# Performance work log

Measured on AMD Instinct MI355X. Metric: run time of the kernel, lower is better.

## Reference

```python
import jax, jax.numpy as jnp
import numpy as np
import math

B, C_IN, C_OUT, K, H = 4, 128, 128, 3, 16
A = C_IN // 8  # attn_dim = in_channels // 8 per 'individual' mode


def setup_inputs() -> dict:
    key = jax.random.key(0)
    ks = jax.random.split(key, 8)
    s = 0.02
    return {
        "x": jax.random.normal(ks[0], (B, C_IN, H, H), jnp.float32),
        "weight": jax.random.normal(ks[1], (C_OUT, C_IN, K, K), jnp.float32) * s,
        "fc_q_w": jax.random.normal(ks[2], (A, C_IN), jnp.float32) * s,
        "fc_q_b": jnp.zeros((A,), jnp.float32),
        "fc_k_w": jax.random.normal(ks[3], (A, 1), jnp.float32) * s,
        "fc_k_b": jnp.zeros((A,), jnp.float32),
        "fc_v_w": jax.random.normal(ks[4], (A, 1), jnp.float32) * s,
        "fc_v_b": jnp.zeros((A,), jnp.float32),
        "fc_o_w": jax.random.normal(ks[5], (1, A), jnp.float32) * s,
        "fc_o_b": jnp.zeros((1,), jnp.float32),
        "gamma": jax.random.normal(ks[6], (1,), jnp.float32),
    }


def reference(x, weight, fc_q_w, fc_q_b, fc_k_w, fc_k_b, fc_v_w, fc_v_b,
              fc_o_w, fc_o_b, gamma):
    b, c_in, h, w_sp = x.shape
    c_out, _, kh, kw = weight.shape
    wflat = weight.reshape(-1)                                 # [Wn]
    xt = x.reshape(b, c_in, -1).transpose(0, 2, 1)             # [B, HW, C_in]
    # AttnOverWeight (mode='individual')
    q = xt @ fc_q_w.T + fc_q_b                                 # [B, HW, A]
    k = wflat[:, None] * fc_k_w[:, 0][None, :] + fc_k_b        # [Wn, A] (Linear(1,A))
    v = wflat[:, None] * fc_v_w[:, 0][None, :] + fc_v_b        # [Wn, A]
    scores = jnp.einsum('bqa,na->bqn', q, k) / math.sqrt(q.shape[-1])
    attn = jax.nn.softmax(scores, axis=2)                      # [B, HW, Wn]
    attn_out = attn.mean(axis=1)[:, :, None] * v[None]         # [B, Wn, A]
    weighted_w = (attn_out @ fc_o_w.T + fc_o_b)[..., 0]        # [B, Wn]
    masked_w = wflat[None, :] + gamma * weighted_w             # [B, Wn]
    # per-sample conv via grouped conv (groups = batch)
    kernels = masked_w.reshape(b * c_out, c_in, kh, kw)
    xg = x.reshape(1, b * c_in, h, w_sp)
    out = jax.lax.conv_general_dilated(
        xg, kernels, window_strides=(1, 1), padding=[(1, 1), (1, 1)],
        feature_group_count=b, dimension_numbers=('NCHW', 'OIHW', 'NCHW'))
    return out.reshape(b, c_out, out.shape[2], out.shape[3])
```

## Files before the change

kernel.cpp:

```cpp
#include <hip/hip_runtime.h>

#define B_      4
#define CIN     128
#define COUT    128
#define HW      256
#define WN      147456
#define WPK     1152
#define ADIM    16

#define WS_G     0
#define WS_G0    128
#define WS_S1    129
#define WS_S0    130
#define WS_BO    131
#define WS_A     132
#define WS_PART  160
#define NBLK_MOM 144
#define MWT_OFF  4096
#define XT_OFF   (4096 + 4*9*128*128*2)

typedef __attribute__((ext_vector_type(8))) short bf16x8;
typedef __attribute__((ext_vector_type(4))) float f32x4;

__device__ __forceinline__ unsigned short f2bf(float f) {
    union { float f; unsigned int u; } v; v.f = f;
    unsigned int u = v.u;
    return (unsigned short)((u + 0x7FFFu + ((u >> 16) & 1u)) >> 16);
}

__device__ __forceinline__ float waveReduceSum(float v) {
    #pragma unroll
    for (int off = 32; off; off >>= 1) v += __shfl_down(v, off, 64);
    return v;
}

__device__ __forceinline__ float blockSum256(float v, float* tmp4, int tid) {
    v = waveReduceSum(v);
    __syncthreads();
    if ((tid & 63) == 0) tmp4[tid >> 6] = v;
    __syncthreads();
    return tmp4[0] + tmp4[1] + tmp4[2] + tmp4[3];
}

__device__ __forceinline__ float blockSum1024(float v, float* tmp16, int tid) {
    v = waveReduceSum(v);
    __syncthreads();
    if ((tid & 63) == 0) tmp16[tid >> 6] = v;
    __syncthreads();
    float s = 0.f;
    #pragma unroll
    for (int i = 0; i < 16; ++i) s += tmp16[i];
    return s;
}

__global__ __launch_bounds__(256) void k_moments(
        const float* __restrict__ w,
        const float* __restrict__ fcq,  const float* __restrict__ fcqb,
        const float* __restrict__ fck,
        const float* __restrict__ fcv,  const float* __restrict__ fcvb,
        const float* __restrict__ fco,  const float* __restrict__ fcob,
        float* __restrict__ ws) {
    __shared__ float tmp4[4];
    const int tid = threadIdx.x, blk = blockIdx.x;

    const float4 w4 = *reinterpret_cast<const float4*>(w + (size_t)(blk * 256 + tid) * 4);
    float m0 = 0.f, m1 = 0.f, m2 = 0.f, m3 = 0.f, m4 = 0.f, m5 = 0.f;
    float vals[4] = {w4.x, w4.y, w4.z, w4.w};
    #pragma unroll
    for (int i = 0; i < 4; ++i) {
        float v = vals[i], v2 = v * v, v3 = v2 * v;
        m0 += v; m1 += v2; m2 += v3; m3 += v2 * v2; m4 += v2 * v3; m5 += v3 * v3;
    }
    float ms[6] = {m0, m1, m2, m3, m4, m5};
    #pragma unroll
    for (int k = 0; k < 6; ++k) {
        float s = blockSum256(ms[k], tmp4, tid);
        if (tid == 0) ws[WS_PART + blk * 6 + k] = s;
    }
    if (blk == 0) {
        if (tid < 128) {
            float s = 0.f;
            #pragma unroll
            for (int a = 0; a < ADIM; ++a) s += fcq[a * CIN + tid] * fck[a];
            ws[WS_G + tid] = s;
        } else if (tid == 128) {
            float s = 0.f;
            for (int a = 0; a < ADIM; ++a) s += fcqb[a] * fck[a];
            ws[WS_G0] = s;
        } else if (tid == 129) {
            float s = 0.f;
            for (int a = 0; a < ADIM; ++a) s += fcv[a] * fco[a];
            ws[WS_S1] = s;
        } else if (tid == 130) {
            float s = 0.f;
            for (int a = 0; a < ADIM; ++a) s += fcvb[a] * fco[a];
            ws[WS_S0] = s;
        } else if (tid == 131) {
            ws[WS_BO] = fcob[0];
        }
    }
}

__global__ __launch_bounds__(1024) void k_alpha(
        const float* __restrict__ x, float* __restrict__ ws) {
    __shared__ float tmp16[16];
    __shared__ float S[7];
    __shared__ float gl[128];
    __shared__ float g0s;
    __shared__ float psum[4][256];
    const int tid = threadIdx.x, b = blockIdx.x;
    const int p = tid & 255, cg = tid >> 8;

    #pragma unroll
    for (int k = 0; k < 6; ++k) {
        float v = (tid < NBLK_MOM) ? ws[WS_PART + tid * 6 + k] : 0.f;
        float s = blockSum1024(v, tmp16, tid);
        if (tid == 0) S[k + 1] = s;
    }
    if (tid < 128) gl[tid] = ws[WS_G + tid];
    if (tid == 128) g0s = ws[WS_G0];
    __syncthreads();

    float dot = 0.f;
    const float* xb = x + (size_t)b * CIN * HW + p;
    const int c0 = cg * 32;
    #pragma unroll 8
    for (int c = 0; c < 32; ++c) dot += xb[(c0 + c) * HW] * gl[c0 + c];
    psum[cg][p] = dot;
    __syncthreads();

    float alpha = 0.f, r = 0.f;
    if (cg == 0) {
        alpha = (psum[0][p] + psum[1][p] + psum[2][p] + psum[3][p] + g0s) * 0.25f;
        float Z = S[6] * (1.f / 720.f);
        Z = Z * alpha + S[5] * (1.f / 120.f);
        Z = Z * alpha + S[4] * (1.f / 24.f);
        Z = Z * alpha + S[3] * (1.f / 6.f);
        Z = Z * alpha + S[2] * 0.5f;
        Z = Z * alpha + S[1];
        Z = Z * alpha + (float)WN;
        r = 1.0f / ((float)HW * Z);
    }
    float t = r;
    const float invk[7] = {1.f, 1.f, 0.5f, 1.f / 3.f, 0.25f, 0.2f, 1.f / 6.f};
    #pragma unroll
    for (int k = 0; k < 7; ++k) {
        float s = blockSum1024(t, tmp16, tid);
        if (tid == 0) ws[WS_A + b * 7 + k] = s;
        t = t * alpha * invk[k + 1 > 6 ? 6 : k + 1];
    }
}

__global__ __launch_bounds__(256) void k_mask(
        const float* __restrict__ w, const float* __restrict__ ws,
        const float* __restrict__ gamma, unsigned short* __restrict__ mwT) {
    const int b = blockIdx.x >> 3, chunk = blockIdx.x & 7;
    const float A0 = ws[WS_A + b * 7 + 0], A1 = ws[WS_A + b * 7 + 1];
    const float A2 = ws[WS_A + b * 7 + 2], A3 = ws[WS_A + b * 7 + 3];
    const float A4 = ws[WS_A + b * 7 + 4], A5 = ws[WS_A + b * 7 + 5];
    const float A6 = ws[WS_A + b * 7 + 6];
    const float s1 = ws[WS_S1], s0 = ws[WS_S0], bo = ws[WS_BO];
    const float gam = gamma[0];

    const int end = chunk * 2048 + 2048;
    for (int i = chunk * 2048 + threadIdx.x; i < end; i += 256) {
        const int co = i >> 7, ci = i & 127;
        const float* wp = w + co * WPK + ci * 9;
        #pragma unroll
        for (int j = 0; j < 9; ++j) {
            float wv = wp[j];
            float pp = A6;
            pp = pp * wv + A5; pp = pp * wv + A4; pp = pp * wv + A3;
            pp = pp * wv + A2; pp = pp * wv + A1; pp = pp * wv + A0;
            float mwv = wv + gam * (pp * (s1 * wv + s0) + bo);
            mwT[(((b * 9 + j) << 7 | co) << 7) | ci] = f2bf(mwv);
        }
    }
}

__global__ __launch_bounds__(256) void k_xt(
        const float* __restrict__ x, unsigned short* __restrict__ xT) {
    const int b = blockIdx.x, tid = threadIdx.x;
    if (tid < 68) {
        int rr, cc;
        if (tid < 18)      { rr = 0;            cc = tid; }
        else if (tid < 36) { rr = 17;           cc = tid - 18; }
        else if (tid < 52) { rr = tid - 36 + 1; cc = 0; }
        else               { rr = tid - 52 + 1; cc = 17; }
        unsigned short* dst = xT + ((size_t)b * 324 + rr * 18 + cc) * 128;
        bf16x8 z = {};
        #pragma unroll
        for (int i = 0; i < 16; ++i) *reinterpret_cast<bf16x8*>(dst + i * 8) = z;
    }
    const int py = tid >> 4, px = tid & 15;
    const float* xb = x + (size_t)b * CIN * HW + tid;
    unsigned short* dst = xT + ((size_t)b * 324 + (py + 1) * 18 + (px + 1)) * 128;
    for (int ci0 = 0; ci0 < 128; ci0 += 8) {
        bf16x8 pk;
        #pragma unroll
        for (int e = 0; e < 8; ++e) pk[e] = (short)f2bf(xb[(ci0 + e) * HW]);
        *reinterpret_cast<bf16x8*>(dst + ci0) = pk;
    }
}

__global__ __launch_bounds__(64) void k_conv_mfma(
        const unsigned short* __restrict__ mwT,
        const unsigned short* __restrict__ xT,
        float* __restrict__ out) {
    const int wgid = blockIdx.x;
    const int l = threadIdx.x;
    const int b = wgid >> 5;
    const int rem = wgid & 31;
    const int cobase = (rem >> 3) * 32;
    const int pbase  = (rem & 7) * 32;
    const int lr = l & 15, lk = l >> 4;

    const int p0 = pbase + lr,       p1 = pbase + 16 + lr;
    const int py0 = p0 >> 4, px0 = p0 & 15;
    const int py1 = p1 >> 4, px1 = p1 & 15;

    f32x4 acc[2][2] = {};

    #pragma unroll 1
    for (int j = 0; j < 9; ++j) {
        const int dy = j / 3, dx = j % 3;
        const unsigned short* ab = mwT + (((b * 9 + j) * 128 + cobase + lr) * 128 + lk * 8);
        const unsigned short* bb0 = xT + (((size_t)b * 324 + (py0 + dy) * 18 + (px0 + dx)) * 128 + lk * 8);
        const unsigned short* bb1 = xT + (((size_t)b * 324 + (py1 + dy) * 18 + (px1 + dx)) * 128 + lk * 8);
        #pragma unroll
        for (int c = 0; c < 4; ++c) {
            bf16x8 a0 = *reinterpret_cast<const bf16x8*>(ab + c * 32);
            bf16x8 a1 = *reinterpret_cast<const bf16x8*>(ab + 16 * 128 + c * 32);
            bf16x8 vb0 = *reinterpret_cast<const bf16x8*>(bb0 + c * 32);
            bf16x8 vb1 = *reinterpret_cast<const bf16x8*>(bb1 + c * 32);
            acc[0][0] = __builtin_amdgcn_mfma_f32_16x16x32_bf16(a0, vb0, acc[0][0], 0, 0, 0);
            acc[0][1] = __builtin_amdgcn_mfma_f32_16x16x32_bf16(a0, vb1, acc[0][1], 0, 0, 0);
            acc[1][0] = __builtin_amdgcn_mfma_f32_16x16x32_bf16(a1, vb0, acc[1][0], 0, 0, 0);
            acc[1][1] = __builtin_amdgcn_mfma_f32_16x16x32_bf16(a1, vb1, acc[1][1], 0, 0, 0);
        }
    }
    #pragma unroll
    for (int s = 0; s < 2; ++s)
        #pragma unroll
        for (int t = 0; t < 2; ++t)
            #pragma unroll
            for (int r = 0; r < 4; ++r) {
                const int co = cobase + s * 16 + lk * 4 + r;
                const int p  = pbase + t * 16 + lr;
                out[((size_t)b * COUT + co) * HW + p] = acc[s][t][r];
            }
}

extern "C" void kernel_launch(void* const* d_in, const int* in_sizes, int n_in,
                              void* d_out, int out_size, void* d_ws, size_t ws_size,
                              hipStream_t stream) {
    const float* x    = (const float*)d_in[0];
    const float* wt   = (const float*)d_in[1];
    const float* fcq  = (const float*)d_in[2];
    const float* fcqb = (const float*)d_in[3];
    const float* fck  = (const float*)d_in[4];
    const float* fcv  = (const float*)d_in[6];
    const float* fcvb = (const float*)d_in[7];
    const float* fco  = (const float*)d_in[8];
    const float* fcob = (const float*)d_in[9];
    const float* gam  = (const float*)d_in[10];
    float* ws  = (float*)d_ws;
    unsigned short* mwT = (unsigned short*)((char*)d_ws + MWT_OFF);
    unsigned short* xT  = (unsigned short*)((char*)d_ws + XT_OFF);
    float* out = (float*)d_out;

    hipLaunchKernelGGL(k_moments, dim3(NBLK_MOM), dim3(256), 0, stream,
                       wt, fcq, fcqb, fck, fcv, fcvb, fco, fcob, ws);
    hipLaunchKernelGGL(k_alpha, dim3(B_), dim3(1024), 0, stream, x, ws);
    hipLaunchKernelGGL(k_mask, dim3(32), dim3(256), 0, stream, wt, ws, gam, mwT);
    hipLaunchKernelGGL(k_xt, dim3(B_), dim3(256), 0, stream, x, xT);
    hipLaunchKernelGGL(k_conv_mfma, dim3(128), dim3(64), 0, stream, mwT, xT, out);
}
```

Measured before the change: 107.4 us.

## Fuse moments into alpha kernel and merge mask/xT kernels to cut launches

Folds the weight moment reduction into the alpha kernel: each of the 4 batch blocks recomputes all moments over the full weight tensor itself instead of reading partials. The mask and input-transpose kernels are merged into one launch, so the pipeline drops from five launches to three. The conv loop over the 9 taps is also unrolled by 3. This removes launch gaps and global round-trips, at the cost of redundant 590KB weight reads in each of only 4 blocks, which serialises that reduction onto few CUs.

```diff
diff --git a/kernel.cpp b/kernel.cpp
--- a/kernel.cpp
+++ b/kernel.cpp
@@ -8,14 +8,10 @@
 #define WPK     1152
 #define ADIM    16
 
-#define WS_G     0
-#define WS_G0    128
-#define WS_S1    129
-#define WS_S0    130
-#define WS_BO    131
-#define WS_A     132
-#define WS_PART  160
-#define NBLK_MOM 144
+#define WS_A     0
+#define WS_S1    28
+#define WS_S0    29
+#define WS_BO    30
 #define MWT_OFF  4096
 #define XT_OFF   (4096 + 4*9*128*128*2)
 
@@ -34,14 +30,6 @@
     return v;
 }
 
-__device__ __forceinline__ float blockSum256(float v, float* tmp4, int tid) {
-    v = waveReduceSum(v);
-    __syncthreads();
-    if ((tid & 63) == 0) tmp4[tid >> 6] = v;
-    __syncthreads();
-    return tmp4[0] + tmp4[1] + tmp4[2] + tmp4[3];
-}
-
 __device__ __forceinline__ float blockSum1024(float v, float* tmp16, int tid) {
     v = waveReduceSum(v);
     __syncthreads();
@@ -53,74 +41,62 @@
     return s;
 }
 
-__global__ __launch_bounds__(256) void k_moments(
-        const float* __restrict__ w,
+__global__ __launch_bounds__(1024) void k_head(
+        const float* __restrict__ x, const float* __restrict__ w,
         const float* __restrict__ fcq,  const float* __restrict__ fcqb,
         const float* __restrict__ fck,
         const float* __restrict__ fcv,  const float* __restrict__ fcvb,
         const float* __restrict__ fco,  const float* __restrict__ fcob,
         float* __restrict__ ws) {
-    __shared__ float tmp4[4];
-    const int tid = threadIdx.x, blk = blockIdx.x;
-
-    const float4 w4 = *reinterpret_cast<const float4*>(w + (size_t)(blk * 256 + tid) * 4);
-    float m0 = 0.f, m1 = 0.f, m2 = 0.f, m3 = 0.f, m4 = 0.f, m5 = 0.f;
-    float vals[4] = {w4.x, w4.y, w4.z, w4.w};
-    #pragma unroll
-    for (int i = 0; i < 4; ++i) {
-        float v = vals[i], v2 = v * v, v3 = v2 * v;
-        m0 += v; m1 += v2; m2 += v3; m3 += v2 * v2; m4 += v2 * v3; m5 += v3 * v3;
-    }
-    float ms[6] = {m0, m1, m2, m3, m4, m5};
-    #pragma unroll
-    for (int k = 0; k < 6; ++k) {
-        float s = blockSum256(ms[k], tmp4, tid);
-        if (tid == 0) ws[WS_PART + blk * 6 + k] = s;
-    }
-    if (blk == 0) {
-        if (tid < 128) {
-            float s = 0.f;
-            #pragma unroll
-            for (int a = 0; a < ADIM; ++a) s += fcq[a * CIN + tid] * fck[a];
-            ws[WS_G + tid] = s;
-        } else if (tid == 128) {
-            float s = 0.f;
-            for (int a = 0; a < ADIM; ++a) s += fcqb[a] * fck[a];
-            ws[WS_G0] = s;
-        } else if (tid == 129) {
-            float s = 0.f;
-            for (int a = 0; a < ADIM; ++a) s += fcv[a] * fco[a];
-            ws[WS_S1] = s;
-        } else if (tid == 130) {
-            float s = 0.f;
-            for (int a = 0; a < ADIM; ++a) s += fcvb[a] * fco[a];
-            ws[WS_S0] = s;
-        } else if (tid == 131) {
-            ws[WS_BO] = fcob[0];
-        }
-    }
-}
-
-__global__ __launch_bounds__(1024) void k_alpha(
-        const float* __restrict__ x, float* __restrict__ ws) {
     __shared__ float tmp16[16];
     __shared__ float S[7];
     __shared__ float gl[128];
     __shared__ float g0s;
     __shared__ float psum[4][256];
     const int tid = threadIdx.x, b = blockIdx.x;
+
+    const float4* w4 = reinterpret_cast<const float4*>(w);
+    float m[6] = {0.f, 0.f, 0.f, 0.f, 0.f, 0.f};
+    #pragma unroll
+    for (int i = 0; i < 36; ++i) {
+        float4 v4 = w4[i * 1024 + tid];
+        float vals[4] = {v4.x, v4.y, v4.z, v4.w};
+        #pragma unroll
+        for (int e = 0; e < 4; ++e) {
+            float v = vals[e], v2 = v * v, v3 = v2 * v;
+            m[0] += v; m[1] += v2; m[2] += v3;
+            m[3] += v2 * v2; m[4] += v2 * v3; m[5] += v3 * v3;
+        }
+    }
+    #pragma unroll
+    for (int k = 0; k < 6; ++k) {
+        float s = blockSum1024(m[k], tmp16, tid);
+        if (tid == 0) S[k + 1] = s;
+    }
+
+    if (tid < 128) {
+        float s = 0.f;
+        #pragma unroll
+        for (int a = 0; a < ADIM; ++a) s += fcq[a * CIN + tid] * fck[a];
+        gl[tid] = s;
+    } else if (tid == 128) {
+        float s = 0.f;
+        for (int a = 0; a < ADIM; ++a) s += fcqb[a] * fck[a];
+        g0s = s;
+    } else if (tid == 129) {
+        float s = 0.f;
+        for (int a = 0; a < ADIM; ++a) s += fcv[a] * fco[a];
+        ws[WS_S1] = s;
+    } else if (tid == 130) {
+        float s = 0.f;
+        for (int a = 0; a < ADIM; ++a) s += fcvb[a] * fco[a];
+        ws[WS_S0] = s;
+    } else if (tid == 131) {
+        ws[WS_BO] = fcob[0];
+    }
+    __syncthreads();
+
     const int p = tid & 255, cg = tid >> 8;
-
-    #pragma unroll
-    for (int k = 0; k < 6; ++k) {
-        float v = (tid < NBLK_MOM) ? ws[WS_PART + tid * 6 + k] : 0.f;
-        float s = blockSum1024(v, tmp16, tid);
-        if (tid == 0) S[k + 1] = s;
-    }
-    if (tid < 128) gl[tid] = ws[WS_G + tid];
-    if (tid == 128) g0s = ws[WS_G0];
-    __syncthreads();
-
     float dot = 0.f;
     const float* xb = x + (size_t)b * CIN * HW + p;
     const int c0 = cg * 32;
@@ -151,55 +127,55 @@
     }
 }
 
-__global__ __launch_bounds__(256) void k_mask(
-        const float* __restrict__ w, const float* __restrict__ ws,
-        const float* __restrict__ gamma, unsigned short* __restrict__ mwT) {
-    const int b = blockIdx.x >> 3, chunk = blockIdx.x & 7;
-    const float A0 = ws[WS_A + b * 7 + 0], A1 = ws[WS_A + b * 7 + 1];
-    const float A2 = ws[WS_A + b * 7 + 2], A3 = ws[WS_A + b * 7 + 3];
-    const float A4 = ws[WS_A + b * 7 + 4], A5 = ws[WS_A + b * 7 + 5];
-    const float A6 = ws[WS_A + b * 7 + 6];
-    const float s1 = ws[WS_S1], s0 = ws[WS_S0], bo = ws[WS_BO];
-    const float gam = gamma[0];
-
-    const int end = chunk * 2048 + 2048;
-    for (int i = chunk * 2048 + threadIdx.x; i < end; i += 256) {
-        const int co = i >> 7, ci = i & 127;
-        const float* wp = w + co * WPK + ci * 9;
-        #pragma unroll
-        for (int j = 0; j < 9; ++j) {
-            float wv = wp[j];
-            float pp = A6;
-            pp = pp * wv + A5; pp = pp * wv + A4; pp = pp * wv + A3;
-            pp = pp * wv + A2; pp = pp * wv + A1; pp = pp * wv + A0;
-            float mwv = wv + gam * (pp * (s1 * wv + s0) + bo);
-            mwT[(((b * 9 + j) << 7 | co) << 7) | ci] = f2bf(mwv);
-        }
-    }
-}
-
-__global__ __launch_bounds__(256) void k_xt(
-        const float* __restrict__ x, unsigned short* __restrict__ xT) {
-    const int b = blockIdx.x, tid = threadIdx.x;
-    if (tid < 68) {
-        int rr, cc;
-        if (tid < 18)      { rr = 0;            cc = tid; }
-        else if (tid < 36) { rr = 17;           cc = tid - 18; }
-        else if (tid < 52) { rr = tid - 36 + 1; cc = 0; }
-        else               { rr = tid - 52 + 1; cc = 17; }
-        unsigned short* dst = xT + ((size_t)b * 324 + rr * 18 + cc) * 128;
-        bf16x8 z = {};
-        #pragma unroll
-        for (int i = 0; i < 16; ++i) *reinterpret_cast<bf16x8*>(dst + i * 8) = z;
-    }
-    const int py = tid >> 4, px = tid & 15;
-    const float* xb = x + (size_t)b * CIN * HW + tid;
-    unsigned short* dst = xT + ((size_t)b * 324 + (py + 1) * 18 + (px + 1)) * 128;
-    for (int ci0 = 0; ci0 < 128; ci0 += 8) {
-        bf16x8 pk;
-        #pragma unroll
-        for (int e = 0; e < 8; ++e) pk[e] = (short)f2bf(xb[(ci0 + e) * HW]);
-        *reinterpret_cast<bf16x8*>(dst + ci0) = pk;
+__global__ __launch_bounds__(256) void k_mx(
+        const float* __restrict__ x, const float* __restrict__ w,
+        const float* __restrict__ ws, const float* __restrict__ gamma,
+        unsigned short* __restrict__ mwT, unsigned short* __restrict__ xT) {
+    const int tid = threadIdx.x;
+    if (blockIdx.x < 32) {
+        const int b = blockIdx.x >> 3, chunk = blockIdx.x & 7;
+        const float A0 = ws[WS_A + b * 7 + 0], A1 = ws[WS_A + b * 7 + 1];
+        const float A2 = ws[WS_A + b * 7 + 2], A3 = ws[WS_A + b * 7 + 3];
+        const float A4 = ws[WS_A + b * 7 + 4], A5 = ws[WS_A + b * 7 + 5];
+        const float A6 = ws[WS_A + b * 7 + 6];
+        const float s1 = ws[WS_S1], s0 = ws[WS_S0], bo = ws[WS_BO];
+        const float gam = gamma[0];
+        const int end = chunk * 2048 + 2048;
+        for (int i = chunk * 2048 + tid; i < end; i += 256) {
+            const int co = i >> 7, ci = i & 127;
+            const float* wp = w + co * WPK + ci * 9;
+            #pragma unroll
+            for (int j = 0; j < 9; ++j) {
+                float wv = wp[j];
+                float pp = A6;
+                pp = pp * wv + A5; pp = pp * wv + A4; pp = pp * wv + A3;
+                pp = pp * wv + A2; pp = pp * wv + A1; pp = pp * wv + A0;
+                float mwv = wv + gam * (pp * (s1 * wv + s0) + bo);
+                mwT[(((b * 9 + j) << 7 | co) << 7) | ci] = f2bf(mwv);
+            }
+        }
+    } else {
+        const int b = blockIdx.x - 32;
+        if (tid < 68) {
+            int rr, cc;
+            if (tid < 18)      { rr = 0;            cc = tid; }
+            else if (tid < 36) { rr = 17;           cc = tid - 18; }
+            else if (tid < 52) { rr = tid - 36 + 1; cc = 0; }
+            else               { rr = tid - 52 + 1; cc = 17; }
+            unsigned short* dst = xT + ((size_t)b * 324 + rr * 18 + cc) * 128;
+            bf16x8 z = {};
+            #pragma unroll
+            for (int i = 0; i < 16; ++i) *reinterpret_cast<bf16x8*>(dst + i * 8) = z;
+        }
+        const int py = tid >> 4, px = tid & 15;
+        const float* xb = x + (size_t)b * CIN * HW + tid;
+        unsigned short* dst = xT + ((size_t)b * 324 + (py + 1) * 18 + (px + 1)) * 128;
+        for (int ci0 = 0; ci0 < 128; ci0 += 8) {
+            bf16x8 pk;
+            #pragma unroll
+            for (int e = 0; e < 8; ++e) pk[e] = (short)f2bf(xb[(ci0 + e) * HW]);
+            *reinterpret_cast<bf16x8*>(dst + ci0) = pk;
+        }
     }
 }
 
@@ -221,7 +197,7 @@
 
     f32x4 acc[2][2] = {};
 
-    #pragma unroll 1
+    #pragma unroll 3
     for (int j = 0; j < 9; ++j) {
         const int dy = j / 3, dx = j % 3;
         const unsigned short* ab = mwT + (((b * 9 + j) * 128 + cobase + lr) * 128 + lk * 8);
@@ -269,10 +245,8 @@
     unsigned short* xT  = (unsigned short*)((char*)d_ws + XT_OFF);
     float* out = (float*)d_out;
 
-    hipLaunchKernelGGL(k_moments, dim3(NBLK_MOM), dim3(256), 0, stream,
-                       wt, fcq, fcqb, fck, fcv, fcvb, fco, fcob, ws);
-    hipLaunchKernelGGL(k_alpha, dim3(B_), dim3(1024), 0, stream, x, ws);
-    hipLaunchKernelGGL(k_mask, dim3(32), dim3(256), 0, stream, wt, ws, gam, mwT);
-    hipLaunchKernelGGL(k_xt, dim3(B_), dim3(256), 0, stream, x, xT);
+    hipLaunchKernelGGL(k_head, dim3(B_), dim3(1024), 0, stream,
+                       x, wt, fcq, fcqb, fck, fcv, fcvb, fco, fcob, ws);
+    hipLaunchKernelGGL(k_mx, dim3(36), dim3(256), 0, stream, x, wt, ws, gam, mwT, xT);
     hipLaunchKernelGGL(k_conv_mfma, dim3(128), dim3(64), 0, stream, mwT, xT, out);
 }
```

Result: slower. 190.4 us (+77.4%).
